# Optimization experiments

Hardware: AMD Instinct MI355X
Metric: run time of the kernel (lower is better)

Reference implementation:

```python
import jax, jax.numpy as jnp
import numpy as np

D_MODEL = 1024
D_K = 1024
D_V = 1024

def setup_inputs() -> dict:
    key = jax.random.key(0)
    k1, k2, k3, k4 = jax.random.split(key, 4)
    X = jax.random.normal(k1, (4, 2048, D_MODEL), dtype=jnp.float32)
    # nn.Linear weights have shape (out_features, in_features)
    s = 1.0 / np.sqrt(D_MODEL)
    W_q = jax.random.uniform(k2, (D_K, D_MODEL), dtype=jnp.float32, minval=-s, maxval=s)
    W_k = jax.random.uniform(k3, (D_K, D_MODEL), dtype=jnp.float32, minval=-s, maxval=s)
    W_v = jax.random.uniform(k4, (D_V, D_MODEL), dtype=jnp.float32, minval=-s, maxval=s)
    return {"X": X, "W_q": W_q, "W_k": W_k, "W_v": W_v}

def reference(X, W_q, W_k, W_v):
    # Q,K,V: [b, m, d]
    Q = jnp.einsum('bmd,kd->bmk', X, W_q)
    K = jnp.einsum('bmd,kd->bmk', X, W_k)
    V = jnp.einsum('bmd,vd->bmv', X, W_v)
    scale = 1.0 / jnp.sqrt(jnp.asarray(D_K, dtype=jnp.float32))
    A = jnp.einsum('bmk,bnk->bmn', Q, K) * scale  # [b, m, m]
    weights = jax.nn.softmax(A, axis=-1)
    context = jnp.einsum('bmn,bnv->bmv', weights, V)
    return (context, weights)
```

## Files before the change

kernel.cpp:

```cpp
#include <hip/hip_runtime.h>
#include <math.h>


typedef __bf16 bf16;
typedef __bf16 bf16x4 __attribute__((ext_vector_type(4)));
typedef __bf16 bf16x8 __attribute__((ext_vector_type(8)));
typedef float  f32x4  __attribute__((ext_vector_type(4)));

#define GLD_TO_LDS(g, l) __builtin_amdgcn_global_load_lds(                    \
    (const __attribute__((address_space(1))) void*)(g),                       \
    (__attribute__((address_space(3))) void*)(l), 16, 0, 0)

#define STAGE_A(tc, P, h) do {                                                \
    const bf16* _s = aRow + (long)((h) * 128) * lda + (long)(tc) * 64;        \
    char* _d = ldsA + (P) * 32768 + (h) * 16384 + t * 16;                     \
    GLD_TO_LDS(_s, _d); GLD_TO_LDS(_s + 64L * lda, _d + 8192); } while (0)
#define STAGE_B(tc, P, h) do {                                                \
    const bf16* _s = bRow + (long)((h) * 128) * ldb + (long)(tc) * 64;        \
    char* _d = ldsB + (P) * 32768 + (h) * 16384 + t * 16;                     \
    GLD_TO_LDS(_s, _d); GLD_TO_LDS(_s + 64L * ldb, _d + 8192); } while (0)
#define VMCNT4 asm volatile("s_waitcnt vmcnt(4)" ::: "memory")

template<int OUT>
__global__ __launch_bounds__(512, 2)
void gemm8(const bf16* __restrict__ A, const bf16* __restrict__ B,
           void* __restrict__ Cp, int nkt, int lda, int ldb, int ldc,
           long sA, long sB, long sC, float alpha)
{
    __shared__ __align__(16) char smem[131072];
    char* ldsA = smem;
    char* ldsB = smem + 65536;

    const int bz = blockIdx.z;
    A += bz * sA;
    B += bz * sB;

    const int t    = threadIdx.x;
    const int wid  = t >> 6;
    const int lane = t & 63;
    const int wr   = wid >> 2;
    const int wn   = wid & 3;
    const int fr   = lane & 15;
    const int g    = lane >> 4;
    const int brow = blockIdx.y * 256;
    const int bcol = blockIdx.x * 256;

    const int  srow = t >> 3;
    const int  scol = ((t & 7) ^ ((t >> 3) & 7)) * 8;
    const bf16* aRow = A + (long)(brow + srow) * lda + scol;
    const bf16* bRow = B + (long)(bcol + srow) * ldb + scol;

    const int  c0  = (g * 16) ^ ((fr & 7) << 4);
    const int  c1  = c0 ^ 64;
    const char* aRd = ldsA + (wr * 128 + fr) * 128;
    const char* bRd = ldsB + (wn * 64 + fr) * 128;

    f32x4 acc[8][4] = {};
    bf16x8 bfrag[4][2];

    STAGE_A(0, 0, 0); STAGE_A(0, 0, 1); STAGE_B(0, 0, 0); STAGE_B(0, 0, 1);
    STAGE_A(1, 1, 0); STAGE_A(1, 1, 1); STAGE_B(1, 1, 0); STAGE_B(1, 1, 1);
    asm volatile("s_waitcnt vmcnt(8)" ::: "memory");
    __builtin_amdgcn_s_barrier();

    const int niter = nkt >> 1;
    for (int it = 0; it < niter; ++it) {
        const int cur = 2 * it;
        const int tc2 = (cur + 2 < nkt) ? cur + 2 : nkt - 1;
        const int tc3 = (cur + 3 < nkt) ? cur + 3 : nkt - 1;
        #pragma unroll
        for (int ph = 0; ph < 8; ++ph) {
            const int q = ph & 3;
            const int P = ph >> 2;

            if (q == 0) {
                #pragma unroll
                for (int n = 0; n < 4; ++n) {
                    bfrag[n][0] = *reinterpret_cast<const bf16x8*>(
                        bRd + P * 32768 + n * 2048 + c0);
                    bfrag[n][1] = *reinterpret_cast<const bf16x8*>(
                        bRd + P * 32768 + n * 2048 + c1);
                }
            }
            bf16x8 af[2][2];
            #pragma unroll
            for (int i = 0; i < 2; ++i) {
                af[i][0] = *reinterpret_cast<const bf16x8*>(
                    aRd + P * 32768 + (2 * q + i) * 2048 + c0);
                af[i][1] = *reinterpret_cast<const bf16x8*>(
                    aRd + P * 32768 + (2 * q + i) * 2048 + c1);
            }

            if (ph == 0) STAGE_A(cur + 1, 1, 0);
            if (ph == 1) STAGE_A(cur + 1, 1, 1);
            if (ph == 2) STAGE_B(tc2, 0, 0);
            if (ph == 3) { STAGE_B(tc2, 0, 1); VMCNT4; }
            if (ph == 4) STAGE_A(tc2, 0, 0);
            if (ph == 5) STAGE_A(tc2, 0, 1);
            if (ph == 6) STAGE_B(tc3, 1, 0);
            if (ph == 7) { STAGE_B(tc3, 1, 1); VMCNT4; }

            __builtin_amdgcn_s_barrier();
            __builtin_amdgcn_s_setprio(1);
            #pragma unroll
            for (int i = 0; i < 2; ++i)
                #pragma unroll
                for (int n = 0; n < 4; ++n) {
                    acc[2 * q + i][n] = __builtin_amdgcn_mfma_f32_16x16x32_bf16(
                        af[i][0], bfrag[n][0], acc[2 * q + i][n], 0, 0, 0);
                    acc[2 * q + i][n] = __builtin_amdgcn_mfma_f32_16x16x32_bf16(
                        af[i][1], bfrag[n][1], acc[2 * q + i][n], 0, 0, 0);
                }
            __builtin_amdgcn_s_setprio(0);
            __builtin_amdgcn_s_barrier();
        }
    }

    #pragma unroll
    for (int m = 0; m < 8; ++m) {
        #pragma unroll
        for (int n = 0; n < 4; ++n) {
            const int ccol = bcol + wn * 64 + n * 16 + fr;
            #pragma unroll
            for (int rr = 0; rr < 4; ++rr) {
                const long crow = brow + wr * 128 + m * 16 + g * 4 + rr;
                const float v = acc[m][n][rr] * alpha;
                if constexpr (OUT == 0) {
                    ((float*)Cp + bz * sC)[crow * ldc + ccol] = v;
                } else {
                    ((bf16*)Cp + bz * sC)[crow * ldc + ccol] = (bf16)v;
                }
            }
        }
    }
}

__global__ __launch_bounds__(256)
void cast_bf16(const float* __restrict__ in, bf16* __restrict__ out, int n4)
{
    int i = blockIdx.x * 256 + threadIdx.x;
    const int stride = gridDim.x * 256;
    for (; i < n4; i += stride) {
        float4 v = reinterpret_cast<const float4*>(in)[i];
        bf16x4 o = { (bf16)v.x, (bf16)v.y, (bf16)v.z, (bf16)v.w };
        reinterpret_cast<bf16x4*>(out)[i] = o;
    }
}

__global__ __launch_bounds__(256)
void softmax_rows(float* __restrict__ W, bf16* __restrict__ Wb)
{
    float* p  = W  + (long)blockIdx.x * 2048;
    bf16*  pb = Wb + (long)blockIdx.x * 2048;
    const int tid  = threadIdx.x;
    const int wid  = tid >> 6;
    const int lane = tid & 63;

    float4 v0 = reinterpret_cast<const float4*>(p)[tid];
    float4 v1 = reinterpret_cast<const float4*>(p)[tid + 256];

    float m = fmaxf(fmaxf(fmaxf(v0.x, v0.y), fmaxf(v0.z, v0.w)),
                    fmaxf(fmaxf(v1.x, v1.y), fmaxf(v1.z, v1.w)));
    #pragma unroll
    for (int off = 32; off >= 1; off >>= 1)
        m = fmaxf(m, __shfl_xor(m, off));

    __shared__ float red[8];
    if (lane == 0) red[wid] = m;
    __syncthreads();
    m = fmaxf(fmaxf(red[0], red[1]), fmaxf(red[2], red[3]));

    v0.x = expf(v0.x - m); v0.y = expf(v0.y - m);
    v0.z = expf(v0.z - m); v0.w = expf(v0.w - m);
    v1.x = expf(v1.x - m); v1.y = expf(v1.y - m);
    v1.z = expf(v1.z - m); v1.w = expf(v1.w - m);

    float s = (v0.x + v0.y + v0.z + v0.w) + (v1.x + v1.y + v1.z + v1.w);
    #pragma unroll
    for (int off = 32; off >= 1; off >>= 1)
        s += __shfl_xor(s, off);
    __syncthreads();
    if (lane == 0) red[4 + wid] = s;
    __syncthreads();
    s = (red[4] + red[5]) + (red[6] + red[7]);

    const float inv = 1.f / s;
    v0.x *= inv; v0.y *= inv; v0.z *= inv; v0.w *= inv;
    v1.x *= inv; v1.y *= inv; v1.z *= inv; v1.w *= inv;
    reinterpret_cast<float4*>(p)[tid]       = v0;
    reinterpret_cast<float4*>(p)[tid + 256] = v1;
    bf16x4 b0 = { (bf16)v0.x, (bf16)v0.y, (bf16)v0.z, (bf16)v0.w };
    bf16x4 b1 = { (bf16)v1.x, (bf16)v1.y, (bf16)v1.z, (bf16)v1.w };
    reinterpret_cast<bf16x4*>(pb)[tid]       = b0;
    reinterpret_cast<bf16x4*>(pb)[tid + 256] = b1;
}

extern "C" void kernel_launch(void* const* d_in, const int* in_sizes, int n_in,
                              void* d_out, int out_size, void* d_ws, size_t ws_size,
                              hipStream_t stream)
{
    const float* X  = (const float*)d_in[0];
    const float* Wq = (const float*)d_in[1];
    const float* Wk = (const float*)d_in[2];
    const float* Wv = (const float*)d_in[3];

    const long BT = 4L * 2048;
    const long D  = 1024;
    const long S  = 2048;
    const long MiB = 1024 * 1024;

    float* ctx = (float*)d_out;
    float* wts = (float*)d_out + BT * D;

    char* ws   = (char*)d_ws;
    bf16* Xb   = (bf16*)(ws);
    bf16* Wqkb = (bf16*)(ws + 16 * MiB);
    bf16* Wvb  = (bf16*)(ws + 20 * MiB);
    bf16* QKb  = (bf16*)(ws + 22 * MiB);
    bf16* Vtb  = (bf16*)(ws + 54 * MiB);
    bf16* Wbf  = (bf16*)(ws);

    dim3 blk(256), blk8(512);

    cast_bf16<<<dim3(2048), blk, 0, stream>>>(X,  Xb,   (int)(BT * D / 4));
    cast_bf16<<<dim3(512),  blk, 0, stream>>>(Wq, Wqkb, (int)(D * D / 4));
    cast_bf16<<<dim3(512),  blk, 0, stream>>>(Wk, Wqkb + D * D, (int)(D * D / 4));
    cast_bf16<<<dim3(512),  blk, 0, stream>>>(Wv, Wvb,  (int)(D * D / 4));

    gemm8<1><<<dim3(8, 32, 1), blk8, 0, stream>>>(Xb, Wqkb, QKb, 16,
                                                  1024, 1024, 2048, 0, 0, 0, 1.f);
    gemm8<1><<<dim3(32, 4, 1), blk8, 0, stream>>>(Wvb, Xb, Vtb, 16,
                                                  1024, 1024, 8192, 0, 0, 0, 1.f);
    gemm8<0><<<dim3(8, 8, 4), blk8, 0, stream>>>(QKb, QKb + 1024, wts, 16,
                                                 2048, 2048, 2048,
                                                 S * 2048, S * 2048, S * S,
                                                 0.03125f);
    softmax_rows<<<dim3(BT), blk, 0, stream>>>(wts, Wbf);

    gemm8<0><<<dim3(4, 8, 4), blk8, 0, stream>>>(Wbf, Vtb, ctx, 32,
                                                 2048, 8192, 1024,
                                                 S * S, S, S * D, 1.f);
}
```

Measured before the change: 309.6 us.

## Split-K the context GEMM with atomic adds, merge weight casts, use fast exp

The final weights×V GEMM (K=2048) is split into two K-halves across blockIdx.z, with each half atomically adding fp32 results into a context buffer that a new kernel zero-fills first. This doubles the grid from 128 to 256 blocks so more CUs stay busy on that GEMM. The three weight-cast launches are merged into one kernel, and softmax uses __expf instead of expf. The cost is extra traffic for the zero-fill and atomics, plus slightly different floating-point rounding.

```diff
diff --git a/kernel.cpp b/kernel.cpp
--- a/kernel.cpp
+++ b/kernel.cpp
@@ -21,19 +21,24 @@
     GLD_TO_LDS(_s, _d); GLD_TO_LDS(_s + 64L * ldb, _d + 8192); } while (0)
 #define VMCNT4 asm volatile("s_waitcnt vmcnt(4)" ::: "memory")
 
-template<int OUT>
+template<int OUT, bool SPLITK>
 __global__ __launch_bounds__(512, 2)
 void gemm8(const bf16* __restrict__ A, const bf16* __restrict__ B,
            void* __restrict__ Cp, int nkt, int lda, int ldb, int ldc,
-           long sA, long sB, long sC, float alpha)
+           long sA, long sB, long sC, long sKa, long sKb, float alpha)
 {
     __shared__ __align__(16) char smem[131072];
     char* ldsA = smem;
     char* ldsB = smem + 65536;
 
-    const int bz = blockIdx.z;
+    const int bz = SPLITK ? (blockIdx.z >> 1) : blockIdx.z;
     A += bz * sA;
     B += bz * sB;
+    if (SPLITK) {
+        const int ck = blockIdx.z & 1;
+        A += ck * sKa;
+        B += ck * sKb;
+    }
 
     const int t    = threadIdx.x;
     const int wid  = t >> 6;
@@ -127,8 +132,10 @@
                 const float v = acc[m][n][rr] * alpha;
                 if constexpr (OUT == 0) {
                     ((float*)Cp + bz * sC)[crow * ldc + ccol] = v;
+                } else if constexpr (OUT == 1) {
+                    ((bf16*)Cp + bz * sC)[crow * ldc + ccol] = (bf16)v;
                 } else {
-                    ((bf16*)Cp + bz * sC)[crow * ldc + ccol] = (bf16)v;
+                    atomicAdd(&((float*)Cp + bz * sC)[crow * ldc + ccol], v);
                 }
             }
         }
@@ -148,6 +155,28 @@
 }
 
 __global__ __launch_bounds__(256)
+void cast_w3(const float* __restrict__ Wq, const float* __restrict__ Wk,
+             const float* __restrict__ Wv, bf16* __restrict__ dst)
+{
+    const int idx = blockIdx.x * 256 + threadIdx.x;
+    const float* src;
+    int off;
+    if (idx < 262144)      { src = Wq; off = idx; }
+    else if (idx < 524288) { src = Wk; off = idx - 262144; }
+    else                   { src = Wv; off = idx - 524288; }
+    float4 v = reinterpret_cast<const float4*>(src)[off];
+    bf16x4 o = { (bf16)v.x, (bf16)v.y, (bf16)v.z, (bf16)v.w };
+    reinterpret_cast<bf16x4*>(dst)[idx] = o;
+}
+
+__global__ __launch_bounds__(256)
+void zerofill(float4* __restrict__ p, int n4)
+{
+    const int i = blockIdx.x * 256 + threadIdx.x;
+    if (i < n4) p[i] = float4{0.f, 0.f, 0.f, 0.f};
+}
+
+__global__ __launch_bounds__(256)
 void softmax_rows(float* __restrict__ W, bf16* __restrict__ Wb)
 {
     float* p  = W  + (long)blockIdx.x * 2048;
@@ -170,10 +199,10 @@
     __syncthreads();
     m = fmaxf(fmaxf(red[0], red[1]), fmaxf(red[2], red[3]));
 
-    v0.x = expf(v0.x - m); v0.y = expf(v0.y - m);
-    v0.z = expf(v0.z - m); v0.w = expf(v0.w - m);
-    v1.x = expf(v1.x - m); v1.y = expf(v1.y - m);
-    v1.z = expf(v1.z - m); v1.w = expf(v1.w - m);
+    v0.x = __expf(v0.x - m); v0.y = __expf(v0.y - m);
+    v0.z = __expf(v0.z - m); v0.w = __expf(v0.w - m);
+    v1.x = __expf(v1.x - m); v1.y = __expf(v1.y - m);
+    v1.z = __expf(v1.z - m); v1.w = __expf(v1.w - m);
 
     float s = (v0.x + v0.y + v0.z + v0.w) + (v1.x + v1.y + v1.z + v1.w);
     #pragma unroll
@@ -222,22 +251,20 @@
 
     dim3 blk(256), blk8(512);
 
-    cast_bf16<<<dim3(2048), blk, 0, stream>>>(X,  Xb,   (int)(BT * D / 4));
-    cast_bf16<<<dim3(512),  blk, 0, stream>>>(Wq, Wqkb, (int)(D * D / 4));
-    cast_bf16<<<dim3(512),  blk, 0, stream>>>(Wk, Wqkb + D * D, (int)(D * D / 4));
-    cast_bf16<<<dim3(512),  blk, 0, stream>>>(Wv, Wvb,  (int)(D * D / 4));
-
-    gemm8<1><<<dim3(8, 32, 1), blk8, 0, stream>>>(Xb, Wqkb, QKb, 16,
-                                                  1024, 1024, 2048, 0, 0, 0, 1.f);
-    gemm8<1><<<dim3(32, 4, 1), blk8, 0, stream>>>(Wvb, Xb, Vtb, 16,
-                                                  1024, 1024, 8192, 0, 0, 0, 1.f);
-    gemm8<0><<<dim3(8, 8, 4), blk8, 0, stream>>>(QKb, QKb + 1024, wts, 16,
-                                                 2048, 2048, 2048,
-                                                 S * 2048, S * 2048, S * S,
-                                                 0.03125f);
+    cast_bf16<<<dim3(2048), blk, 0, stream>>>(X, Xb, (int)(BT * D / 4));
+    cast_w3<<<dim3(3072), blk, 0, stream>>>(Wq, Wk, Wv, Wqkb);
+    zerofill<<<dim3(8192), blk, 0, stream>>>((float4*)ctx, (int)(BT * D / 4));
+
+    gemm8<1, false><<<dim3(8, 32, 1), blk8, 0, stream>>>(
+        Xb, Wqkb, QKb, 16, 1024, 1024, 2048, 0, 0, 0, 0, 0, 1.f);
+    gemm8<1, false><<<dim3(32, 4, 1), blk8, 0, stream>>>(
+        Wvb, Xb, Vtb, 16, 1024, 1024, 8192, 0, 0, 0, 0, 0, 1.f);
+    gemm8<0, false><<<dim3(8, 8, 4), blk8, 0, stream>>>(
+        QKb, QKb + 1024, wts, 16, 2048, 2048, 2048,
+        S * 2048, S * 2048, S * S, 0, 0, 0.03125f);
     softmax_rows<<<dim3(BT), blk, 0, stream>>>(wts, Wbf);
 
-    gemm8<0><<<dim3(4, 8, 4), blk8, 0, stream>>>(Wbf, Vtb, ctx, 32,
-                                                 2048, 8192, 1024,
-                                                 S * S, S, S * D, 1.f);
-}
+    gemm8<2, true><<<dim3(4, 8, 8), blk8, 0, stream>>>(
+        Wbf, Vtb, ctx, 16, 2048, 8192, 1024,
+        S * S, S, S * D, 1024, 1024, 1.f);
+}
```

New measurement: 344.5 us. 11.3% more time.
